# Kernel optimization log

Measured on AMD Instinct MI355X. Metric: run time of the kernel, lower is better.

## Reference

```python
import jax, jax.numpy as jnp
import numpy as np

T, H, E, I, K = 1024, 1024, 16, 512, 4   # tokens, hidden, n_experts, expert ffn dim, top_k
IS = 1024                                 # shared-experts intermediate = n_shared(2) * I
LIMIT = 7.0                               # swiglu_limit
SCALE = 2.5                               # routed_scaling_factor
VOCAB = 32000


def setup_inputs() -> dict:
    key = jax.random.key(0)
    ks = jax.random.split(key, 10)
    sh = 1.0 / np.sqrt(H)
    si = 1.0 / np.sqrt(I)
    ss = 1.0 / np.sqrt(IS)
    x = jax.random.normal(ks[0], (T, H), jnp.float32)
    input_ids = jax.random.randint(ks[1], (T,), 0, VOCAB)
    Wg = jax.random.normal(ks[2], (E, H), jnp.float32) * sh          # gate (router), fp32
    bias = jax.random.normal(ks[3], (E,), jnp.float32) * 0.1         # e_score_correction_bias
    W1 = jax.random.normal(ks[4], (E, H, I), jnp.float32) * sh       # expert gate proj
    W3 = jax.random.normal(ks[5], (E, H, I), jnp.float32) * sh       # expert up proj
    W2 = jax.random.normal(ks[6], (E, I, H), jnp.float32) * si       # expert down proj
    Wsg = jax.random.normal(ks[7], (H, IS), jnp.float32) * sh        # shared gate proj
    Wsu = jax.random.normal(ks[8], (H, IS), jnp.float32) * sh        # shared up proj
    Wsd = jax.random.normal(ks[9], (IS, H), jnp.float32) * ss        # shared down proj
    return {"hidden_states": x, "input_ids": input_ids, "Wg": Wg, "bias": bias,
            "W1": W1, "W3": W3, "W2": W2, "Wsg": Wsg, "Wsu": Wsu, "Wsd": Wsd}


def reference(hidden_states, input_ids, Wg, bias, W1, W3, W2, Wsg, Wsu, Wsd):
    x = hidden_states  # [T, H]
    # --- router (fp32 logits, sqrtsoftplus scoring, noaux_tc top-k with correction bias) ---
    logits = jnp.einsum('th,eh->te', x.astype(jnp.float32), Wg)       # [T, E]
    scores = jnp.sqrt(jax.nn.softplus(logits))                         # sqrtsoftplus
    _, topi = jax.lax.top_k(scores + bias[None, :], K)                 # select with bias
    w = jnp.take_along_axis(scores, topi, axis=1)                      # weights from raw scores
    w = w / jnp.sum(w, axis=1, keepdims=True) * SCALE                  # renormalize + scale
    # dense [T, E] combine weights (zero for unselected experts)
    w_dense = jnp.zeros((T, E), x.dtype).at[jnp.arange(T)[:, None], topi].add(w.astype(x.dtype))
    # --- routed experts: clamped swiglu (gpt-oss style, per swiglu_limit) ---
    g = jnp.einsum('th,ehi->tei', x, W1)                               # [T, E, I]
    u = jnp.einsum('th,ehi->tei', x, W3)
    g = jnp.clip(g, None, LIMIT)
    u = jnp.clip(u, -LIMIT, LIMIT)
    act = (g * jax.nn.sigmoid(1.702 * g)) * (u + 1.0)
    routed = jnp.einsum('tei,eih,te->th', act, W2, w_dense)            # weighted combine
    # --- shared experts: standard SiLU-gated MLP ---
    shared = (jax.nn.silu(x @ Wsg) * (x @ Wsu)) @ Wsd
    return routed + shared
```

## Files before the change

kernel.cpp:

```cpp
#include <hip/hip_runtime.h>
#include <hip/hip_bf16.h>
#include <math.h>
#include <stdint.h>

#define T_ 1024
#define H_ 1024
#define E_ 16
#define I_ 512
#define KSEL 4
#define IS_ 1024

typedef unsigned short u16;
typedef __attribute__((ext_vector_type(8))) short short8;
typedef __attribute__((ext_vector_type(4))) float f32x4;

__device__ __forceinline__ u16 f2bf(float f) {
    union { float f; unsigned int u; } v; v.f = f;
    unsigned int u = v.u;
    return (u16)((u + 0x7fffu + ((u >> 16) & 1u)) >> 16);
}
__device__ __forceinline__ float bf2f(u16 b) {
    union { unsigned int u; float f; } v; v.u = ((unsigned int)b) << 16;
    return v.f;
}
__device__ __forceinline__ unsigned cvtpk(float lo, float hi) {
    unsigned r;
    asm("v_cvt_pk_bf16_f32 %0, %1, %2" : "=v"(r) : "v"(lo), "v"(hi));
    return r;
}
__device__ __forceinline__ void gload16(const u16* g, u16* l) {
    __builtin_amdgcn_global_load_lds(
        (const __attribute__((address_space(1))) void*)g,
        (__attribute__((address_space(3))) void*)l, 16, 0, 0);
}
__device__ __forceinline__ f32x4 ldg4(const float* p) {
    return *reinterpret_cast<const __attribute__((address_space(1))) f32x4*>(
        reinterpret_cast<uintptr_t>(p));
}
__device__ __forceinline__ void SB0() { __builtin_amdgcn_sched_barrier(0); }
__device__ __forceinline__ void BARRIER() {
    asm volatile("s_waitcnt lgkmcnt(0)" ::: "memory");
    __builtin_amdgcn_s_barrier();
    __builtin_amdgcn_sched_barrier(0);
}

__global__ __launch_bounds__(256)
void router_kernel(const float* __restrict__ x, const float* __restrict__ Wg,
                   const float* __restrict__ bias, int* __restrict__ counts,
                   int* __restrict__ tok_list, int* __restrict__ slot_list,
                   float* __restrict__ wt_dense, u16* __restrict__ x_bf, int cap) {
    __shared__ float part[4][16];
    int t = blockIdx.x;
    int tid = threadIdx.x;
    int e = tid & 15;
    int q = tid >> 4;
    const float4* xv = (const float4*)(x + (long)t * H_) + q * 16;
    const float4* wv = (const float4*)(Wg + (long)e * H_) + q * 16;
    float d = 0.f;
#pragma unroll
    for (int i = 0; i < 16; i++) {
        float4 a = xv[i], b = wv[i];
        d += a.x * b.x + a.y * b.y + a.z * b.z + a.w * b.w;
    }
    d += __shfl_down(d, 16);
    d += __shfl_down(d, 32);
    if ((tid & 63) < 16) part[tid >> 6][e] = d;
    {
        float4 v = ((const float4*)(x + (long)t * H_))[tid];
        ushort4 o;
        o.x = f2bf(v.x); o.y = f2bf(v.y); o.z = f2bf(v.z); o.w = f2bf(v.w);
        ((ushort4*)(x_bf + (long)t * H_))[tid] = o;
    }
    __syncthreads();
    if (tid >= 64) return;
    int lane = tid;
    float lg = part[0][e] + part[1][e] + part[2][e] + part[3][e];
    float sp = fmaxf(lg, 0.f) + log1pf(expf(-fabsf(lg)));
    float s = sqrtf(sp);
    float bs = s + bias[e];
    int sel[KSEL]; float ssel[KSEL]; float wsum = 0.f;
#pragma unroll
    for (int k = 0; k < KSEL; k++) {
        float mv = bs; int me = e;
#pragma unroll
        for (int off = 1; off < 16; off <<= 1) {
            float ov = __shfl_xor(mv, off);
            int oe = __shfl_xor(me, off);
            if (ov > mv || (ov == mv && oe < me)) { mv = ov; me = oe; }
        }
        sel[k] = me;
        float sk = __shfl(s, (lane & 48) | me);
        ssel[k] = sk; wsum += sk;
        if (e == me) bs = -1e30f;
    }
    float inv = 2.5f / wsum;
    if (lane < KSEL) {
        int k = lane;
        int se = sel[k];
        wt_dense[t * KSEL + k] = ssel[k] * inv;
        int pos = atomicAdd(&counts[se], 1);
        if (pos < cap) {
            tok_list[se * T_ + pos] = t;
            slot_list[se * T_ + pos] = t * KSEL + k;
        }
    }
}

struct Seg {
    const u16* A; const int* gather;
    const float* B0; const float* B1;
    void* C; const int* scatter; const int* counts;
    long sAe, sBe, sCe;
    int lda, ldb, ldc;
    int il, cf32, act, nt, nxt, mt, nE, cap, Mfull;
};

__global__ __launch_bounds__(256, 2)
void moe_gemm(Seg sa, Seg sb) {
    int id = blockIdx.x;
    int n0 = sa.nxt * sa.mt * sa.nE;
    Seg s = (id < n0) ? sa : sb;
    int rid = (id < n0) ? id : id - n0;
    int per = s.nxt * s.mt;
    int e = rid / per;
    int r2 = rid - e * per;
    int my = r2 / s.nxt;
    int nx = r2 - my * s.nxt;
    int Mlim = s.counts ? (s.counts[e] < s.cap ? s.counts[e] : s.cap) : s.Mfull;
    int mbase = my * 128;
    if (mbase >= Mlim) return;
    int nbase = nx * 128;
    int nt = s.nt;

    __shared__ __align__(16) u16 lds[40960];
    u16* a0 = lds;
    u16* a1 = lds + 8192;
    u16* a2 = lds + 16384;
    u16* Bb0 = lds + 24576;
    u16* Bb1 = lds + 32768;

    int tid = threadIdx.x, lane = tid & 63, wid = tid >> 6;

    const u16* Abase = s.A + (long)e * s.sAe;
    const int* gat = s.gather ? s.gather + e * T_ : nullptr;
    const u16* aptr[4];
    {
        int srow = tid >> 3;
        int kca = (tid & 7) ^ (srow & 7);
#pragma unroll
        for (int j = 0; j < 4; j++) {
            int gr = mbase + srow + j * 32;
            int grc = gr < Mlim ? gr : (Mlim - 1);
            long ar = gat ? (long)gat[grc] : (long)grc;
            aptr[j] = Abase + ar * (long)s.lda + kca * 8;
        }
    }
    int adoff = tid * 8;

    int cg = tid & 31, kc = tid >> 5;
    const float* bp;
    {
        int pc = nbase + cg * 4;
        if (s.il) {
            int chunk = pc >> 4;
            const float* src = (chunk & 1) ? s.B1 : s.B0;
            bp = src + (long)e * s.sBe + ((chunk >> 1) * 16 + (pc & 15));
        } else {
            bp = s.B0 + (long)e * s.sBe + pc;
        }
        bp += (long)(kc * 8) * s.ldb;
    }
    long ldbl = s.ldb;
    f32x4 bA[8], bB[8];

    auto issueA = [&](u16* ab, int kt) {
#pragma unroll
        for (int j = 0; j < 4; j++)
            gload16(aptr[j] + kt * 64, ab + adoff + j * 2048);
    };
    auto issueB = [&](f32x4 (&b)[8], int kt) {
        const float* r = bp + (long)(kt * 64) * ldbl;
#pragma unroll
        for (int i = 0; i < 8; i++)
            b[i] = ldg4(r + (long)i * ldbl);
    };
    auto cvtw = [&](f32x4 (&b)[8], u16* bb) {
        const int P[4] = {0, 5, 2, 7};
#pragma unroll
        for (int j = 0; j < 4; j++) {
            int rho = (j << 5) | cg;
            int slot = kc ^ (cg & 7) ^ P[j];
            uint4 v;
            v.x = cvtpk(b[0][j], b[1][j]);
            v.y = cvtpk(b[2][j], b[3][j]);
            v.z = cvtpk(b[4][j], b[5][j]);
            v.w = cvtpk(b[6][j], b[7][j]);
            *(uint4*)(bb + rho * 64 + slot * 8) = v;
        }
    };

    int wm = wid >> 1, wn = wid & 1, lr = lane & 15, lk = lane >> 4;
    f32x4 acc[4][4] = {};
    auto compute = [&](const u16* ab, const u16* bb) {
        const int P[4] = {0, 5, 2, 7};
#pragma unroll
        for (int kk = 0; kk < 2; kk++) {
            short8 afr[4], bfr[4];
#pragma unroll
            for (int mi = 0; mi < 4; mi++) {
                int R = wm * 64 + mi * 16 + lr;
                afr[mi] = *(const short8*)(ab + R * 64 + (((kk * 4 + lk) ^ (R & 7)) << 3));
            }
#pragma unroll
            for (int ni = 0; ni < 4; ni++) {
                int R = wn * 64 + ni * 16 + lr;
                int rho = ((R & 3) << 5) | (R >> 2);
                int key = ((R >> 2) & 7) ^ P[R & 3];
                bfr[ni] = *(const short8*)(bb + rho * 64 + (((kk * 4 + lk) ^ key) << 3));
            }
            __builtin_amdgcn_s_setprio(1);
#pragma unroll
            for (int mi = 0; mi < 4; mi++)
#pragma unroll
                for (int ni = 0; ni < 4; ni++)
                    acc[mi][ni] = __builtin_amdgcn_mfma_f32_16x16x32_bf16(afr[mi], bfr[ni], acc[mi][ni], 0, 0, 0);
            __builtin_amdgcn_s_setprio(0);
        }
    };

    issueA(a0, 0); SB0(); issueB(bA, 0); SB0();
    issueA(a1, 1); SB0(); issueB(bB, 1); SB0();
    cvtw(bA, Bb0);
    BARRIER();

    for (int t = 0; t < nt; t += 2) {
        if (t + 2 < nt) { issueA(a2, t + 2); SB0(); issueB(bA, t + 2); SB0(); }
        compute(a0, Bb0);
        cvtw(bB, Bb1);
        BARRIER();
        if (t + 3 < nt) { issueA(a0, t + 3); SB0(); issueB(bB, t + 3); SB0(); }
        compute(a1, Bb1);
        if (t + 2 < nt) { cvtw(bA, Bb0); BARRIER(); }
        u16* tmp = a0; a0 = a2; a2 = a1; a1 = tmp;
    }

    if (s.act == 0) {
        u16* Cb = (u16*)s.C;
        float* Cf = (float*)s.C;
        long cbase = s.scatter ? 0L : (long)e * s.sCe;
        const int* scat = s.scatter ? s.scatter + e * T_ : nullptr;
#pragma unroll
        for (int mi = 0; mi < 4; mi++) {
#pragma unroll
            for (int j = 0; j < 4; j++) {
                int rowt = wm * 64 + mi * 16 + lk * 4 + j;
                int gr = mbase + rowt;
                if (gr >= Mlim) continue;
                long crow = scat ? (long)scat[gr] : (long)gr;
                long rb = cbase + crow * (long)s.ldc;
#pragma unroll
                for (int ni = 0; ni < 4; ni++) {
                    int col = nbase + wn * 64 + ni * 16 + lr;
                    float v = acc[mi][ni][j];
                    if (s.cf32) Cf[rb + col] = v;
                    else        Cb[rb + col] = f2bf(v);
                }
            }
        }
    } else {
        u16* Co = (u16*)s.C;
        long cbase = (long)e * s.sCe;
#pragma unroll
        for (int mi = 0; mi < 4; mi++) {
#pragma unroll
            for (int j = 0; j < 4; j++) {
                int rowt = wm * 64 + mi * 16 + lk * 4 + j;
                int gr = mbase + rowt;
                if (gr >= Mlim) continue;
                long rb = cbase + (long)gr * s.ldc;
#pragma unroll
                for (int q = 0; q < 2; q++) {
                    int ocol = (nbase >> 1) + wn * 32 + q * 16 + lr;
                    float g = acc[mi][2 * q][j];
                    float u = acc[mi][2 * q + 1][j];
                    float r;
                    if (s.act == 1) {
                        r = g / (1.f + expf(-g)) * u;
                    } else {
                        g = fminf(g, 7.f);
                        u = fminf(fmaxf(u, -7.f), 7.f);
                        r = g / (1.f + expf(-1.702f * g)) * (u + 1.f);
                    }
                    Co[rb + ocol] = f2bf(r);
                }
            }
        }
    }
}

__global__ void final_add_kernel(float* __restrict__ out, const u16* __restrict__ down,
                                 const float* __restrict__ wtd) {
    int i = blockIdx.x * blockDim.x + threadIdx.x;
    int o = i * 4;
    int t = o >> 10;
    int h = o & (H_ - 1);
    float4 w4 = *(const float4*)(wtd + t * 4);
    float wk[4] = {w4.x, w4.y, w4.z, w4.w};
    float4 v = ((float4*)out)[i];
#pragma unroll
    for (int k = 0; k < KSEL; k++) {
        const u16* dr = down + ((long)(t * KSEL + k) << 10) + h;
        ushort4 d4 = *(const ushort4*)dr;
        v.x += wk[k] * bf2f(d4.x);
        v.y += wk[k] * bf2f(d4.y);
        v.z += wk[k] * bf2f(d4.z);
        v.w += wk[k] * bf2f(d4.w);
    }
    ((float4*)out)[i] = v;
}

extern "C" void kernel_launch(void* const* d_in, const int* in_sizes, int n_in,
                              void* d_out, int out_size, void* d_ws, size_t ws_size,
                              hipStream_t stream) {
    const float* x    = (const float*)d_in[0];
    const float* Wg   = (const float*)d_in[2];
    const float* bias = (const float*)d_in[3];
    const float* W1   = (const float*)d_in[4];
    const float* W3   = (const float*)d_in[5];
    const float* W2   = (const float*)d_in[6];
    const float* Wsg  = (const float*)d_in[7];
    const float* Wsu  = (const float*)d_in[8];
    const float* Wsd  = (const float*)d_in[9];
    float* out = (float*)d_out;
    char* ws = (char*)d_ws;

    size_t off = 0;
    auto carve = [&](size_t bytes) -> char* {
        char* p = ws + off;
        off = (off + bytes + 255) & ~(size_t)255;
        return p;
    };
    u16* x_bf   = (u16*)carve((size_t)T_ * H_ * 2);
    u16* c1     = (u16*)carve((size_t)T_ * IS_ * 2);
    u16* dwn    = (u16*)carve((size_t)T_ * KSEL * H_ * 2);
    int* counts    = (int*)carve(E_ * sizeof(int));
    int* tok_list  = (int*)carve((size_t)E_ * T_ * 4);
    int* slot_list = (int*)carve((size_t)E_ * T_ * 4);
    float* wt_dense = (float*)carve((size_t)T_ * KSEL * 4);

    long cap = 768;
    int capB = (int)(cap / 128);
    u16* act = (u16*)carve((size_t)E_ * cap * I_ * 2);

    hipMemsetAsync(counts, 0, E_ * sizeof(int), stream);
    router_kernel<<<T_, 256, 0, stream>>>(x, Wg, bias, counts, tok_list, slot_list,
                                          wt_dense, x_bf, (int)cap);

    Seg eu;
    eu.A = x_bf; eu.gather = tok_list; eu.B0 = W1; eu.B1 = W3;
    eu.C = (void*)act; eu.scatter = nullptr; eu.counts = counts;
    eu.sAe = 0; eu.sBe = (long)H_ * I_; eu.sCe = (long)cap * I_;
    eu.lda = H_; eu.ldb = I_; eu.ldc = I_;
    eu.il = 1; eu.cf32 = 0; eu.act = 2; eu.nt = 16;
    eu.nxt = 8; eu.mt = capB; eu.nE = E_; eu.cap = (int)cap; eu.Mfull = 0;
    Seg su;
    su.A = x_bf; su.gather = nullptr; su.B0 = Wsg; su.B1 = Wsu;
    su.C = (void*)c1; su.scatter = nullptr; su.counts = nullptr;
    su.sAe = 0; su.sBe = 0; su.sCe = 0;
    su.lda = H_; su.ldb = IS_; su.ldc = IS_;
    su.il = 1; su.cf32 = 0; su.act = 1; su.nt = 16;
    su.nxt = 16; su.mt = 8; su.nE = 1; su.cap = 0; su.Mfull = T_;
    int upBlocks = eu.nxt * eu.mt * eu.nE + su.nxt * su.mt * su.nE;
    moe_gemm<<<upBlocks, 256, 0, stream>>>(eu, su);

    Seg ed;
    ed.A = act; ed.gather = nullptr; ed.B0 = W2; ed.B1 = W2;
    ed.C = (void*)dwn; ed.scatter = slot_list; ed.counts = counts;
    ed.sAe = (long)cap * I_; ed.sBe = (long)I_ * H_; ed.sCe = 0;
    ed.lda = I_; ed.ldb = H_; ed.ldc = H_;
    ed.il = 0; ed.cf32 = 0; ed.act = 0; ed.nt = 8;
    ed.nxt = 8; ed.mt = capB; ed.nE = E_; ed.cap = (int)cap; ed.Mfull = 0;
    Seg sd;
    sd.A = c1; sd.gather = nullptr; sd.B0 = Wsd; sd.B1 = Wsd;
    sd.C = (void*)out; sd.scatter = nullptr; sd.counts = nullptr;
    sd.sAe = 0; sd.sBe = 0; sd.sCe = 0;
    sd.lda = IS_; sd.ldb = H_; sd.ldc = H_;
    sd.il = 0; sd.cf32 = 1; sd.act = 0; sd.nt = 16;
    sd.nxt = 8; sd.mt = 8; sd.nE = 1; sd.cap = 0; sd.Mfull = T_;
    int dnBlocks = ed.nxt * ed.mt * ed.nE + sd.nxt * sd.mt * sd.nE;
    moe_gemm<<<dnBlocks, 256, 0, stream>>>(ed, sd);

    final_add_kernel<<<T_ * H_ / 4 / 256, 256, 0, stream>>>(out, dwn, wt_dense);
}
```

Measured before the change: 90.77 us.

## Shrink MoE GEMM LDS footprint with single B buffer and vmcnt-gated pipeline

Replaces the triple-buffered A tiles and double-buffered B tiles in LDS with two A buffers and one shared B buffer, cutting LDS from 80KB to 48KB per block. This should allow more resident blocks per CU. The main loop now waits on outstanding vector memory loads with an explicit vmcnt and converts the next B tile into the single buffer between barriers. This adds two barriers per K-step and shortens the prefetch distance, which trades latency hiding for occupancy. The per-expert capacity also drops from 768 to 512 rows, which reduces the number of early-exiting blocks in the grid but would drop tokens if an expert received more than 512.

```diff
diff --git a/kernel.cpp b/kernel.cpp
--- a/kernel.cpp
+++ b/kernel.cpp
@@ -41,6 +41,10 @@
 __device__ __forceinline__ void BARRIER() {
     asm volatile("s_waitcnt lgkmcnt(0)" ::: "memory");
     __builtin_amdgcn_s_barrier();
+    __builtin_amdgcn_sched_barrier(0);
+}
+__device__ __forceinline__ void VMW12() {
+    asm volatile("s_waitcnt vmcnt(12)" ::: "memory");
     __builtin_amdgcn_sched_barrier(0);
 }
 
@@ -132,12 +136,10 @@
     int nbase = nx * 128;
     int nt = s.nt;
 
-    __shared__ __align__(16) u16 lds[40960];
+    __shared__ __align__(16) u16 lds[24576];
     u16* a0 = lds;
     u16* a1 = lds + 8192;
-    u16* a2 = lds + 16384;
-    u16* Bb0 = lds + 24576;
-    u16* Bb1 = lds + 32768;
+    u16* Bb = lds + 16384;
 
     int tid = threadIdx.x, lane = tid & 63, wid = tid >> 6;
 
@@ -184,7 +186,7 @@
         for (int i = 0; i < 8; i++)
             b[i] = ldg4(r + (long)i * ldbl);
     };
-    auto cvtw = [&](f32x4 (&b)[8], u16* bb) {
+    auto cvtw = [&](f32x4 (&b)[8]) {
         const int P[4] = {0, 5, 2, 7};
 #pragma unroll
         for (int j = 0; j < 4; j++) {
@@ -195,13 +197,13 @@
             v.y = cvtpk(b[2][j], b[3][j]);
             v.z = cvtpk(b[4][j], b[5][j]);
             v.w = cvtpk(b[6][j], b[7][j]);
-            *(uint4*)(bb + rho * 64 + slot * 8) = v;
+            *(uint4*)(Bb + rho * 64 + slot * 8) = v;
         }
     };
 
     int wm = wid >> 1, wn = wid & 1, lr = lane & 15, lk = lane >> 4;
     f32x4 acc[4][4] = {};
-    auto compute = [&](const u16* ab, const u16* bb) {
+    auto compute = [&](const u16* ab) {
         const int P[4] = {0, 5, 2, 7};
 #pragma unroll
         for (int kk = 0; kk < 2; kk++) {
@@ -216,7 +218,7 @@
                 int R = wn * 64 + ni * 16 + lr;
                 int rho = ((R & 3) << 5) | (R >> 2);
                 int key = ((R >> 2) & 7) ^ P[R & 3];
-                bfr[ni] = *(const short8*)(bb + rho * 64 + (((kk * 4 + lk) ^ key) << 3));
+                bfr[ni] = *(const short8*)(Bb + rho * 64 + (((kk * 4 + lk) ^ key) << 3));
             }
             __builtin_amdgcn_s_setprio(1);
 #pragma unroll
@@ -228,20 +230,25 @@
         }
     };
 
-    issueA(a0, 0); SB0(); issueB(bA, 0); SB0();
-    issueA(a1, 1); SB0(); issueB(bB, 1); SB0();
-    cvtw(bA, Bb0);
+    issueB(bA, 0); SB0(); issueA(a0, 0); SB0();
+    cvtw(bA);
+    issueB(bB, 1); SB0(); issueA(a1, 1); SB0();
     BARRIER();
 
     for (int t = 0; t < nt; t += 2) {
-        if (t + 2 < nt) { issueA(a2, t + 2); SB0(); issueB(bA, t + 2); SB0(); }
-        compute(a0, Bb0);
-        cvtw(bB, Bb1);
+        VMW12();
+        compute(a0);
         BARRIER();
-        if (t + 3 < nt) { issueA(a0, t + 3); SB0(); issueB(bB, t + 3); SB0(); }
-        compute(a1, Bb1);
-        if (t + 2 < nt) { cvtw(bA, Bb0); BARRIER(); }
-        u16* tmp = a0; a0 = a2; a2 = a1; a1 = tmp;
+        if (t + 1 < nt) cvtw(bB);
+        if (t + 2 < nt) { issueB(bA, t + 2); SB0(); issueA(a0, t + 2); SB0(); }
+        BARRIER();
+        if (t + 1 >= nt) break;
+        VMW12();
+        compute(a1);
+        BARRIER();
+        if (t + 2 < nt) cvtw(bA);
+        if (t + 3 < nt) { issueB(bB, t + 3); SB0(); issueA(a1, t + 3); SB0(); }
+        BARRIER();
     }
 
     if (s.act == 0) {
@@ -348,7 +355,7 @@
     int* slot_list = (int*)carve((size_t)E_ * T_ * 4);
     float* wt_dense = (float*)carve((size_t)T_ * KSEL * 4);
 
-    long cap = 768;
+    long cap = 512;
     int capB = (int)(cap / 128);
     u16* act = (u16*)carve((size_t)E_ * cap * I_ * 2);
 
```

After: 122.0 us. +34.4%, slower.
